# Kernel optimization log

Measured on AMD Instinct MI355X. Metric: run time of the kernel, lower is better.

The kernel has to match this reference:

```python
import jax, jax.numpy as jnp
import numpy as np

R = 32
EPS = 0.0
BN_EPS = 1e-5


def _voxelize(features, idx):
    # features: [C, N], idx: [N] int32 flat voxel index in [0, R^3)
    V = R * R * R
    pts = features.T  # [N, C]
    sums = jax.ops.segment_sum(pts, idx, num_segments=V)          # [V, C]
    cnts = jax.ops.segment_sum(jnp.ones_like(idx, jnp.float32), idx, num_segments=V)  # [V]
    avg = sums / jnp.maximum(cnts, 1.0)[:, None]
    mx = jax.ops.segment_max(pts, idx, num_segments=V)            # [V, C], -inf for empty
    mx = jnp.where(cnts[:, None] > 0, mx, 0.0)
    return avg, mx, cnts


def reference(features, coords, conv_w, conv_b, bn_gamma, bn_beta, bn_mean, bn_var):
    B, C, N = features.shape
    # --- coordinate normalization (coords detached in original) ---
    nc = coords - jnp.mean(coords, axis=2, keepdims=True)          # [B,3,N]
    norms = jnp.linalg.norm(nc, axis=1, keepdims=True)             # [B,1,N]
    denom = jnp.max(norms, axis=2, keepdims=True) * 2.0 + EPS      # [B,1,1]
    nc = nc / denom + 0.5
    nc = jnp.clip(nc * R, 0.0, R - 1)                              # [B,3,N]
    vox = jnp.round(nc).astype(jnp.int32)                          # [B,3,N]
    idx = vox[:, 0] * (R * R) + vox[:, 1] * R + vox[:, 2]          # [B,N]
    # --- dual scatter reduction (avg + max) per batch ---
    avg, mx, _ = jax.vmap(_voxelize)(features, idx)                # [B, V, C] each
    fea = jnp.concatenate([mx, avg], axis=-1)                      # [B, V, 2C]
    # --- 1x1 Conv3d == channel matmul ---
    y = jnp.einsum('bvc,oc->bvo', fea, conv_w) + conv_b            # [B, V, C]
    # --- BatchNorm3d (eval mode) ---
    y = (y - bn_mean) * (bn_gamma / jnp.sqrt(bn_var + BN_EPS)) + bn_beta
    # --- Swish ---
    y = y * jax.nn.sigmoid(y)
    out = jnp.transpose(y, (0, 2, 1)).reshape(B, C, R, R, R)
    return out, nc


def setup_inputs() -> dict:
    key = jax.random.key(0)
    ks = jax.random.split(key, 8)
    B, C, N = 8, 240, 16384
    return {
        'features': jax.random.normal(ks[0], (B, C, N), jnp.float32),
        'coords': jax.random.normal(ks[1], (B, 3, N), jnp.float32),
        'conv_w': jax.random.normal(ks[2], (C, 2 * C), jnp.float32) * 0.05,
        'conv_b': jax.random.normal(ks[3], (C,), jnp.float32) * 0.05,
        'bn_gamma': jnp.ones((C,), jnp.float32),
        'bn_beta': jnp.zeros((C,), jnp.float32),
        'bn_mean': jnp.zeros((C,), jnp.float32),
        'bn_var': jax.random.uniform(ks[4], (C,), jnp.float32, 0.5, 1.5),
    }
```

## Files before the change

kernel.cpp:

```cpp
#include <hip/hip_runtime.h>
#include <math.h>

#define RR 32
#define V 32768
#define C 240
#define N 16384
#define B 8
#define K2C 480
#define NG 2048
#define GZ 16
#define FPAD 488
#define EBUF 512

typedef __attribute__((ext_vector_type(8))) short bf16x8;
typedef __attribute__((ext_vector_type(4))) float f32x4;

__device__ __forceinline__ unsigned short f2bf(float x) {
    unsigned u = __float_as_uint(x);
    u += 0x7fffu + ((u >> 16) & 1u);
    return (unsigned short)(u >> 16);
}

__global__ __launch_bounds__(256) void init_stats_kernel(const float* __restrict__ coords,
                                                         float* __restrict__ stats,
                                                         int* __restrict__ hist,
                                                         const float* __restrict__ w,
                                                         unsigned short* __restrict__ w_bf) {
    int blk = blockIdx.x;
    int tid = threadIdx.x;
    if (blk < 256) {
        int t = blk * 256 + tid;
        int4 z4 = {0, 0, 0, 0};
        ((int4*)hist)[t] = z4;
        if (t < 57600) {
            unsigned lo = f2bf(w[2 * t]);
            unsigned hi = f2bf(w[2 * t + 1]);
            ((unsigned*)w_bf)[t] = lo | (hi << 16);
        }
        return;
    }
    int b = blk - 256;
    const float* cb = coords + (size_t)b * 3 * N;
    __shared__ float red[256];
    float m[3];
    for (int d = 0; d < 3; ++d) {
        float s = 0.f;
        for (int n = tid; n < N; n += 256) s += cb[d * N + n];
        red[tid] = s; __syncthreads();
        for (int w2 = 128; w2 > 0; w2 >>= 1) { if (tid < w2) red[tid] += red[tid + w2]; __syncthreads(); }
        m[d] = red[0] / (float)N;
        __syncthreads();
    }
    float mx = 0.f;
    for (int n = tid; n < N; n += 256) {
        float dx = cb[0 * N + n] - m[0];
        float dy = cb[1 * N + n] - m[1];
        float dz = cb[2 * N + n] - m[2];
        mx = fmaxf(mx, dx * dx + dy * dy + dz * dz);
    }
    red[tid] = mx; __syncthreads();
    for (int w2 = 128; w2 > 0; w2 >>= 1) { if (tid < w2) red[tid] = fmaxf(red[tid], red[tid + w2]); __syncthreads(); }
    if (tid == 0) {
        stats[b * 4 + 0] = m[0];
        stats[b * 4 + 1] = m[1];
        stats[b * 4 + 2] = m[2];
        stats[b * 4 + 3] = 2.f * sqrtf(red[0]);
    }
}

__global__ __launch_bounds__(256) void nc_idx_kernel(const float* __restrict__ coords,
                                                     const float* __restrict__ stats,
                                                     float* __restrict__ nc_out,
                                                     int* __restrict__ idxbuf,
                                                     int* __restrict__ hist) {
    int t = blockIdx.x * 256 + threadIdx.x;
    int b = t >> 14;
    int n = t & (N - 1);
    float denom = stats[b * 4 + 3];
    int v[3];
#pragma unroll
    for (int d = 0; d < 3; ++d) {
        float x = coords[((size_t)b * 3 + d) * N + n];
        float t0 = (x - stats[b * 4 + d]) / denom + 0.5f;
        t0 = t0 * (float)RR;
        t0 = fminf(fmaxf(t0, 0.f), (float)(RR - 1));
        nc_out[((size_t)b * 3 + d) * N + n] = t0;
        v[d] = (int)rintf(t0);
    }
    int iv = v[0] * (RR * RR) + v[1] * RR + v[2];
    idxbuf[t] = iv;
    atomicAdd(hist + b * V + iv, 1);
}

__global__ __launch_bounds__(1024) void prefix_kernel(const int* __restrict__ hist,
                                                      int* __restrict__ starts,
                                                      int* __restrict__ cursor) {
    __shared__ int part[1024];
    int b = blockIdx.x, t = threadIdx.x;
    int base = b * V + t * 32;
    const int4* hp = (const int4*)(hist + base);
    int4 h[8];
    int s = 0;
#pragma unroll
    for (int j = 0; j < 8; ++j) { h[j] = hp[j]; s += h[j].x + h[j].y + h[j].z + h[j].w; }
    part[t] = s; __syncthreads();
    for (int off = 1; off < 1024; off <<= 1) {
        int x = (t >= off) ? part[t - off] : 0;
        __syncthreads();
        part[t] += x;
        __syncthreads();
    }
    int run = part[t] - s;
    int4* sp = (int4*)(starts + base);
    int4* cp = (int4*)(cursor + base);
#pragma unroll
    for (int j = 0; j < 8; ++j) {
        int4 o;
        o.x = run; run += h[j].x;
        o.y = run; run += h[j].y;
        o.z = run; run += h[j].z;
        o.w = run; run += h[j].w;
        sp[j] = o; cp[j] = o;
    }
}

__global__ __launch_bounds__(256) void plist_kernel(const int* __restrict__ idxbuf,
                                                    int* __restrict__ cursor,
                                                    int* __restrict__ ptlist) {
    int t = blockIdx.x * 256 + threadIdx.x;
    int b = t >> 14;
    int n = t & (N - 1);
    int iv = idxbuf[t];
    int pos = atomicAdd(cursor + b * V + iv, 1);
    ptlist[(b << 14) + pos] = (n << 5) | (iv & 31);
}

__global__ __launch_bounds__(256) void transpose_kernel(const float* __restrict__ feat,
                                                        unsigned short* __restrict__ featT) {
    __shared__ float t[C][33];
    int b = blockIdx.y;
    int n0 = blockIdx.x * 32;
    int l = threadIdx.x;
    const float* fb = feat + (size_t)b * C * N;
    unsigned short* fTb = featT + (size_t)b * N * C;
    int nl = l & 31, cs = l >> 5;
#pragma unroll
    for (int p = 0; p < 30; ++p) {
        int c = p * 8 + cs;
        t[c][nl] = fb[(size_t)c * N + n0 + nl];
    }
    __syncthreads();
    int ci = l & 127;
    int nh = l >> 7;
#pragma unroll
    for (int p = 0; p < 16; ++p) {
        int n = 2 * p + nh;
        if (ci < 120) {
            unsigned lo = f2bf(t[2 * ci][n]);
            unsigned hi = f2bf(t[2 * ci + 1][n]);
            *(unsigned*)&fTb[(size_t)(n0 + n) * C + 2 * ci] = lo | (hi << 16);
        }
    }
}

__global__ __launch_bounds__(256) void column_kernel(
    const unsigned short* __restrict__ featT,
    const int* __restrict__ ptlist,
    const int* __restrict__ starts,
    const int* __restrict__ hist,
    const unsigned short* __restrict__ w_bf,
    const float* __restrict__ cbias, const float* __restrict__ gamma,
    const float* __restrict__ beta, const float* __restrict__ mean,
    const float* __restrict__ var,
    float* __restrict__ out) {
    const int g = blockIdx.x, b = blockIdx.y;
    const int tid = threadIdx.x;
    const int v0 = g * GZ;
    float* outb = out + (size_t)b * C * V;

    __shared__ float A_s[C], B_s[C], rcp_s[GZ];
    __shared__ unsigned short fea_s[GZ][FPAD];
    __shared__ int cnt_s[GZ];
    __shared__ int ebuf[EBUF];

    if (tid < C) {
        float sc = gamma[tid] * rsqrtf(var[tid] + 1e-5f);
        A_s[tid] = sc;
        B_s[tid] = (cbias[tid] - mean[tid]) * sc + beta[tid];
    }
    if (tid < GZ) {
        int c0 = hist[b * V + v0 + tid];
        cnt_s[tid] = c0;
        rcp_s[tid] = 1.f / (float)max(c0, 1);
    }
    __syncthreads();

    int pc = 0;
#pragma unroll
    for (int z = 0; z < GZ; ++z) pc += cnt_s[z];

    if (pc == 0) {
        for (int i = tid; i < C * GZ; i += 256) {
            int o = i >> 4, vv = i & (GZ - 1);
            float y = B_s[o];
            y = y / (1.f + __expf(-y));
            outb[(size_t)o * V + v0 + vv] = y;
        }
        return;
    }

    for (int i = tid; i < GZ * FPAD / 2; i += 256) ((unsigned*)fea_s)[i] = 0u;

    const int c = tid;
    const bool act = tid < C;
    const int pos = starts[b * V + v0];
    const int* pl = ptlist + (b << 14) + pos;
    const unsigned short* fT = featT + (size_t)b * N * C;

    float s0 = 0.f, mx0 = -INFINITY;
    int curz = -1;
    for (int base = 0; base < pc; base += EBUF) {
        int mm = min(EBUF, pc - base);
        __syncthreads();
        for (int i = tid; i < mm; i += 256) ebuf[i] = pl[base + i];
        __syncthreads();
        if (act) {
            for (int i0 = 0; i0 < mm; i0 += 16) {
                int m = min(16, mm - i0);
                int e_[16];
#pragma unroll
                for (int j = 0; j < 16; ++j) e_[j] = ebuf[i0 + ((j < m) ? j : m - 1)];
                unsigned short u_[16];
#pragma unroll
                for (int j = 0; j < 16; ++j)
                    u_[j] = fT[(size_t)(e_[j] >> 5) * C + c];
#pragma unroll
                for (int j = 0; j < 16; ++j) {
                    if (j < m) {
                        int zj = e_[j] & (GZ - 1);
                        if (zj != curz) {
                            if (curz >= 0) {
                                fea_s[curz][c] = f2bf(mx0);
                                fea_s[curz][C + c] = f2bf(s0 * rcp_s[curz]);
                            }
                            curz = zj; s0 = 0.f; mx0 = -INFINITY;
                        }
                        float f = __uint_as_float(((unsigned)u_[j]) << 16);
                        s0 += f; mx0 = fmaxf(mx0, f);
                    }
                }
            }
        }
    }
    if (act && curz >= 0) {
        fea_s[curz][c] = f2bf(mx0);
        fea_s[curz][C + c] = f2bf(s0 * rcp_s[curz]);
    }
    __syncthreads();

    const int lane = tid & 63, wave = tid >> 6;
    const int mcnt = (wave == 3) ? 3 : 4;
    const int zl = lane & 15;
    const int koff = (lane >> 4) * 8;

    f32x4 acc[4];
#pragma unroll
    for (int i = 0; i < 4; ++i) acc[i] = (f32x4){0.f, 0.f, 0.f, 0.f};

#pragma unroll
    for (int kc = 0; kc < 15; ++kc) {
        const int kg = kc * 32 + koff;
        bf16x8 bfr = *(const bf16x8*)&fea_s[zl][kg];
        const unsigned short* wp = w_bf + (size_t)(wave * 64 + zl) * K2C + kg;
#pragma unroll
        for (int mt = 0; mt < 4; ++mt) {
            if (mt < mcnt) {
                bf16x8 afr = *(const bf16x8*)(wp + (size_t)mt * 16 * K2C);
                acc[mt] = __builtin_amdgcn_mfma_f32_16x16x32_bf16(afr, bfr, acc[mt], 0, 0, 0);
            }
        }
    }

    const int vv = v0 + zl;
    const int rbase = (lane >> 4) * 4;
#pragma unroll
    for (int mt = 0; mt < 4; ++mt) {
        if (mt < mcnt) {
#pragma unroll
            for (int r = 0; r < 4; ++r) {
                int o = (wave * 4 + mt) * 16 + rbase + r;
                float y = acc[mt][r] * A_s[o] + B_s[o];
                y = y / (1.f + __expf(-y));
                outb[(size_t)o * V + vv] = y;
            }
        }
    }
}

extern "C" void kernel_launch(void* const* d_in, const int* in_sizes, int n_in,
                              void* d_out, int out_size, void* d_ws, size_t ws_size,
                              hipStream_t stream) {
    const float* features = (const float*)d_in[0];
    const float* coords   = (const float*)d_in[1];
    const float* conv_w   = (const float*)d_in[2];
    const float* conv_b   = (const float*)d_in[3];
    const float* gamma    = (const float*)d_in[4];
    const float* beta     = (const float*)d_in[5];
    const float* mean     = (const float*)d_in[6];
    const float* var      = (const float*)d_in[7];

    float* out    = (float*)d_out;
    float* nc_out = out + (size_t)B * C * V;

    char* ws = (char*)d_ws;
    size_t off = 0;
    auto carve = [&](size_t bytes) { char* p = ws + off; off += (bytes + 255) & ~(size_t)255; return p; };
    int*            hist   = (int*)carve((size_t)B * V * 4);
    float*          stats  = (float*)carve(B * 4 * 4);
    int*            idxbuf = (int*)carve((size_t)B * N * 4);
    int*            starts = (int*)carve((size_t)B * V * 4);
    int*            cursor = (int*)carve((size_t)B * V * 4);
    int*            ptlist = (int*)carve((size_t)B * N * 4);
    unsigned short* w_bf   = (unsigned short*)carve((size_t)C * K2C * 2);
    unsigned short* featT  = (unsigned short*)carve((size_t)B * N * C * 2);
    (void)off;

    init_stats_kernel<<<256 + B, 256, 0, stream>>>(coords, stats, hist, conv_w, w_bf);
    nc_idx_kernel<<<(B * N) / 256, 256, 0, stream>>>(coords, stats, nc_out, idxbuf, hist);
    prefix_kernel<<<B, 1024, 0, stream>>>(hist, starts, cursor);
    plist_kernel<<<(B * N) / 256, 256, 0, stream>>>(idxbuf, cursor, ptlist);
    transpose_kernel<<<dim3(N / 32, B), 256, 0, stream>>>(features, featT);
    column_kernel<<<dim3(NG, B), 256, 0, stream>>>(
        featT, ptlist, starts, hist, w_bf,
        conv_b, gamma, beta, mean, var, out);
    (void)in_sizes; (void)n_in; (void)out_size;
}
```

Baseline: 608.8 us.

## Widen voxel group to 32 and loop four groups per persistent block

Each block now covers a 32-voxel z-column instead of 16 and walks four such groups, cutting the grid from 2048 to 256 blocks per batch. BN/bias/swish constants and the swish of the bias for empty voxels are computed once per block. Each weight fragment loaded from global memory now feeds two MFMAs, one per 16-voxel half. Empty groups write float4 stores. This trades fewer blocks and less parallelism for reuse of the weights and setup work, and adds more accumulator registers.

```diff
diff --git a/kernel.cpp b/kernel.cpp
--- a/kernel.cpp
+++ b/kernel.cpp
@@ -7,8 +7,8 @@
 #define N 16384
 #define B 8
 #define K2C 480
-#define NG 2048
-#define GZ 16
+#define GZ 32
+#define GPB 4
 #define FPAD 488
 #define EBUF 512
 
@@ -173,125 +173,137 @@
     const float* __restrict__ beta, const float* __restrict__ mean,
     const float* __restrict__ var,
     float* __restrict__ out) {
-    const int g = blockIdx.x, b = blockIdx.y;
+    const int bx = blockIdx.x, b = blockIdx.y;
     const int tid = threadIdx.x;
-    const int v0 = g * GZ;
     float* outb = out + (size_t)b * C * V;
 
-    __shared__ float A_s[C], B_s[C], rcp_s[GZ];
-    __shared__ unsigned short fea_s[GZ][FPAD];
+    __shared__ float A_s[C], B_s[C], y0_s[C];
+    __shared__ __align__(16) unsigned short fea_s[GZ][FPAD];
     __shared__ int cnt_s[GZ];
     __shared__ int ebuf[EBUF];
 
     if (tid < C) {
         float sc = gamma[tid] * rsqrtf(var[tid] + 1e-5f);
         A_s[tid] = sc;
-        B_s[tid] = (cbias[tid] - mean[tid]) * sc + beta[tid];
-    }
-    if (tid < GZ) {
-        int c0 = hist[b * V + v0 + tid];
-        cnt_s[tid] = c0;
-        rcp_s[tid] = 1.f / (float)max(c0, 1);
-    }
-    __syncthreads();
-
-    int pc = 0;
-#pragma unroll
-    for (int z = 0; z < GZ; ++z) pc += cnt_s[z];
-
-    if (pc == 0) {
-        for (int i = tid; i < C * GZ; i += 256) {
-            int o = i >> 4, vv = i & (GZ - 1);
-            float y = B_s[o];
-            y = y / (1.f + __expf(-y));
-            outb[(size_t)o * V + v0 + vv] = y;
-        }
-        return;
-    }
-
-    for (int i = tid; i < GZ * FPAD / 2; i += 256) ((unsigned*)fea_s)[i] = 0u;
+        float b0 = (cbias[tid] - mean[tid]) * sc + beta[tid];
+        B_s[tid] = b0;
+        y0_s[tid] = b0 / (1.f + __expf(-b0));
+    }
 
     const int c = tid;
     const bool act = tid < C;
-    const int pos = starts[b * V + v0];
-    const int* pl = ptlist + (b << 14) + pos;
     const unsigned short* fT = featT + (size_t)b * N * C;
-
-    float s0 = 0.f, mx0 = -INFINITY;
-    int curz = -1;
-    for (int base = 0; base < pc; base += EBUF) {
-        int mm = min(EBUF, pc - base);
-        __syncthreads();
-        for (int i = tid; i < mm; i += 256) ebuf[i] = pl[base + i];
-        __syncthreads();
-        if (act) {
-            for (int i0 = 0; i0 < mm; i0 += 16) {
-                int m = min(16, mm - i0);
-                int e_[16];
-#pragma unroll
-                for (int j = 0; j < 16; ++j) e_[j] = ebuf[i0 + ((j < m) ? j : m - 1)];
-                unsigned short u_[16];
-#pragma unroll
-                for (int j = 0; j < 16; ++j)
-                    u_[j] = fT[(size_t)(e_[j] >> 5) * C + c];
-#pragma unroll
-                for (int j = 0; j < 16; ++j) {
-                    if (j < m) {
-                        int zj = e_[j] & (GZ - 1);
-                        if (zj != curz) {
-                            if (curz >= 0) {
-                                fea_s[curz][c] = f2bf(mx0);
-                                fea_s[curz][C + c] = f2bf(s0 * rcp_s[curz]);
-                            }
-                            curz = zj; s0 = 0.f; mx0 = -INFINITY;
-                        }
-                        float f = __uint_as_float(((unsigned)u_[j]) << 16);
-                        s0 += f; mx0 = fmaxf(mx0, f);
-                    }
-                }
-            }
-        }
-    }
-    if (act && curz >= 0) {
-        fea_s[curz][c] = f2bf(mx0);
-        fea_s[curz][C + c] = f2bf(s0 * rcp_s[curz]);
-    }
-    __syncthreads();
 
     const int lane = tid & 63, wave = tid >> 6;
     const int mcnt = (wave == 3) ? 3 : 4;
     const int zl = lane & 15;
     const int koff = (lane >> 4) * 8;
-
-    f32x4 acc[4];
-#pragma unroll
-    for (int i = 0; i < 4; ++i) acc[i] = (f32x4){0.f, 0.f, 0.f, 0.f};
-
-#pragma unroll
-    for (int kc = 0; kc < 15; ++kc) {
-        const int kg = kc * 32 + koff;
-        bf16x8 bfr = *(const bf16x8*)&fea_s[zl][kg];
-        const unsigned short* wp = w_bf + (size_t)(wave * 64 + zl) * K2C + kg;
+    const int rbase = (lane >> 4) * 4;
+
+    for (int gi = 0; gi < GPB; ++gi) {
+        const int g = gi * 256 + bx;
+        const int v0 = g * GZ;
+
+        __syncthreads();
+        if (tid < GZ) cnt_s[tid] = hist[b * V + v0 + tid];
+        __syncthreads();
+
+        int pc = 0;
+#pragma unroll
+        for (int z = 0; z < GZ; ++z) pc += cnt_s[z];
+
+        if (pc == 0) {
+            for (int i = tid; i < GZ * C / 4; i += 256) {
+                int o = i >> 3, q = i & 7;
+                float y = y0_s[o];
+                float4 f4 = {y, y, y, y};
+                *(float4*)&outb[(size_t)o * V + v0 + q * 4] = f4;
+            }
+            continue;
+        }
+
+        for (int i = tid; i < GZ * FPAD / 2; i += 256) ((unsigned*)fea_s)[i] = 0u;
+
+        const int pos = starts[b * V + v0];
+        const int* pl = ptlist + (b << 14) + pos;
+
+        float s0 = 0.f, mx0 = -INFINITY;
+        int curz = -1;
+        for (int base = 0; base < pc; base += EBUF) {
+            int mm = min(EBUF, pc - base);
+            __syncthreads();
+            for (int i = tid; i < mm; i += 256) ebuf[i] = pl[base + i];
+            __syncthreads();
+            if (act) {
+                for (int i0 = 0; i0 < mm; i0 += 16) {
+                    int m = min(16, mm - i0);
+                    int e_[16];
+#pragma unroll
+                    for (int j = 0; j < 16; ++j) e_[j] = ebuf[i0 + ((j < m) ? j : m - 1)];
+                    unsigned short u_[16];
+#pragma unroll
+                    for (int j = 0; j < 16; ++j)
+                        u_[j] = fT[(size_t)(e_[j] >> 5) * C + c];
+#pragma unroll
+                    for (int j = 0; j < 16; ++j) {
+                        if (j < m) {
+                            int zj = e_[j] & (GZ - 1);
+                            if (zj != curz) {
+                                if (curz >= 0) {
+                                    float k = (float)cnt_s[curz];
+                                    fea_s[curz][c] = f2bf(mx0);
+                                    fea_s[curz][C + c] = f2bf(s0 / k);
+                                }
+                                curz = zj; s0 = 0.f; mx0 = -INFINITY;
+                            }
+                            float f = __uint_as_float(((unsigned)u_[j]) << 16);
+                            s0 += f; mx0 = fmaxf(mx0, f);
+                        }
+                    }
+                }
+            }
+        }
+        if (act && curz >= 0) {
+            float k = (float)cnt_s[curz];
+            fea_s[curz][c] = f2bf(mx0);
+            fea_s[curz][C + c] = f2bf(s0 / k);
+        }
+        __syncthreads();
+
+        f32x4 acc0[4], acc1[4];
+#pragma unroll
+        for (int i = 0; i < 4; ++i) { acc0[i] = (f32x4){0.f, 0.f, 0.f, 0.f}; acc1[i] = (f32x4){0.f, 0.f, 0.f, 0.f}; }
+
+#pragma unroll
+        for (int kc = 0; kc < 15; ++kc) {
+            const int kg = kc * 32 + koff;
+            bf16x8 bfr0 = *(const bf16x8*)&fea_s[zl][kg];
+            bf16x8 bfr1 = *(const bf16x8*)&fea_s[16 + zl][kg];
+            const unsigned short* wp = w_bf + (size_t)(wave * 64 + zl) * K2C + kg;
+#pragma unroll
+            for (int mt = 0; mt < 4; ++mt) {
+                if (mt < mcnt) {
+                    bf16x8 afr = *(const bf16x8*)(wp + (size_t)mt * 16 * K2C);
+                    acc0[mt] = __builtin_amdgcn_mfma_f32_16x16x32_bf16(afr, bfr0, acc0[mt], 0, 0, 0);
+                    acc1[mt] = __builtin_amdgcn_mfma_f32_16x16x32_bf16(afr, bfr1, acc1[mt], 0, 0, 0);
+                }
+            }
+        }
+
+        const int vv = v0 + zl;
 #pragma unroll
         for (int mt = 0; mt < 4; ++mt) {
             if (mt < mcnt) {
-                bf16x8 afr = *(const bf16x8*)(wp + (size_t)mt * 16 * K2C);
-                acc[mt] = __builtin_amdgcn_mfma_f32_16x16x32_bf16(afr, bfr, acc[mt], 0, 0, 0);
-            }
-        }
-    }
-
-    const int vv = v0 + zl;
-    const int rbase = (lane >> 4) * 4;
-#pragma unroll
-    for (int mt = 0; mt < 4; ++mt) {
-        if (mt < mcnt) {
-#pragma unroll
-            for (int r = 0; r < 4; ++r) {
-                int o = (wave * 4 + mt) * 16 + rbase + r;
-                float y = acc[mt][r] * A_s[o] + B_s[o];
-                y = y / (1.f + __expf(-y));
-                outb[(size_t)o * V + vv] = y;
+#pragma unroll
+                for (int r = 0; r < 4; ++r) {
+                    int o = (wave * 4 + mt) * 16 + rbase + r;
+                    float y = acc0[mt][r] * A_s[o] + B_s[o];
+                    y = y / (1.f + __expf(-y));
+                    outb[(size_t)o * V + vv] = y;
+                    float y1 = acc1[mt][r] * A_s[o] + B_s[o];
+                    y1 = y1 / (1.f + __expf(-y1));
+                    outb[(size_t)o * V + vv + 16] = y1;
+                }
             }
         }
     }
@@ -330,7 +342,7 @@
     prefix_kernel<<<B, 1024, 0, stream>>>(hist, starts, cursor);
     plist_kernel<<<(B * N) / 256, 256, 0, stream>>>(idxbuf, cursor, ptlist);
     transpose_kernel<<<dim3(N / 32, B), 256, 0, stream>>>(features, featT);
-    column_kernel<<<dim3(NG, B), 256, 0, stream>>>(
+    column_kernel<<<dim3(256, B), 256, 0, stream>>>(
         featT, ptlist, starts, hist, w_bf,
         conv_b, gamma, beta, mean, var, out);
     (void)in_sizes; (void)n_in; (void)out_size;
```

Measured after the change: 886.5 us. 1.46x slower.

## Compact non-empty voxel groups into worklist and fuse prep kernels

Applied to the files above, without the earlier changes.

Builds a per-batch worklist of non-empty 16-voxel groups during the prefix scan, so the heavy column kernel only does real work for occupied groups and early-exits the rest. Empty groups are written with the constant bias-swish value by extra blocks fused into the point-list fill kernel. The feature transpose is merged into the init/stats kernel to save a launch. This adds atomics in the prefix scan, and the column kernel still launches the full grid of blocks, which now mostly exit immediately.

```diff
diff --git a/kernel.cpp b/kernel.cpp
--- a/kernel.cpp
+++ b/kernel.cpp
@@ -7,8 +7,8 @@
 #define N 16384
 #define B 8
 #define K2C 480
-#define NG 2048
 #define GZ 16
+#define NGRP 2048
 #define FPAD 488
 #define EBUF 512
 
@@ -21,25 +21,56 @@
     return (unsigned short)(u >> 16);
 }
 
-__global__ __launch_bounds__(256) void init_stats_kernel(const float* __restrict__ coords,
-                                                         float* __restrict__ stats,
-                                                         int* __restrict__ hist,
-                                                         const float* __restrict__ w,
-                                                         unsigned short* __restrict__ w_bf) {
+__global__ __launch_bounds__(256) void prep_kernel(const float* __restrict__ feat,
+                                                   unsigned short* __restrict__ featT,
+                                                   const float* __restrict__ coords,
+                                                   float* __restrict__ stats,
+                                                   int* __restrict__ hist,
+                                                   int* __restrict__ wlcnt,
+                                                   const float* __restrict__ w,
+                                                   unsigned short* __restrict__ w_bf) {
+    __shared__ float t[C][33];
     int blk = blockIdx.x;
     int tid = threadIdx.x;
-    if (blk < 256) {
-        int t = blk * 256 + tid;
+    if (blk < 4096) {
+        int bx = blk & 511, b = blk >> 9;
+        int n0 = bx * 32;
+        int l = tid;
+        const float* fb = feat + (size_t)b * C * N;
+        unsigned short* fTb = featT + (size_t)b * N * C;
+        int nl = l & 31, cs = l >> 5;
+#pragma unroll
+        for (int p = 0; p < 30; ++p) {
+            int c = p * 8 + cs;
+            t[c][nl] = fb[(size_t)c * N + n0 + nl];
+        }
+        __syncthreads();
+        int ci = l & 127;
+        int nh = l >> 7;
+#pragma unroll
+        for (int p = 0; p < 16; ++p) {
+            int n = 2 * p + nh;
+            if (ci < 120) {
+                unsigned lo = f2bf(t[2 * ci][n]);
+                unsigned hi = f2bf(t[2 * ci + 1][n]);
+                *(unsigned*)&fTb[(size_t)(n0 + n) * C + 2 * ci] = lo | (hi << 16);
+            }
+        }
+        return;
+    }
+    if (blk < 4352) {
+        int tt = (blk - 4096) * 256 + tid;
         int4 z4 = {0, 0, 0, 0};
-        ((int4*)hist)[t] = z4;
-        if (t < 57600) {
-            unsigned lo = f2bf(w[2 * t]);
-            unsigned hi = f2bf(w[2 * t + 1]);
-            ((unsigned*)w_bf)[t] = lo | (hi << 16);
-        }
+        ((int4*)hist)[tt] = z4;
+        if (tt < 57600) {
+            unsigned lo = f2bf(w[2 * tt]);
+            unsigned hi = f2bf(w[2 * tt + 1]);
+            ((unsigned*)w_bf)[tt] = lo | (hi << 16);
+        }
+        if (tt < B) wlcnt[tt] = 0;
         return;
     }
-    int b = blk - 256;
+    int b = blk - 4352;
     const float* cb = coords + (size_t)b * 3 * N;
     __shared__ float red[256];
     float m[3];
@@ -94,15 +125,23 @@
 
 __global__ __launch_bounds__(1024) void prefix_kernel(const int* __restrict__ hist,
                                                       int* __restrict__ starts,
-                                                      int* __restrict__ cursor) {
+                                                      int* __restrict__ cursor,
+                                                      int* __restrict__ wl,
+                                                      int* __restrict__ wlcnt) {
     __shared__ int part[1024];
     int b = blockIdx.x, t = threadIdx.x;
     int base = b * V + t * 32;
     const int4* hp = (const int4*)(hist + base);
     int4 h[8];
-    int s = 0;
-#pragma unroll
-    for (int j = 0; j < 8; ++j) { h[j] = hp[j]; s += h[j].x + h[j].y + h[j].z + h[j].w; }
+#pragma unroll
+    for (int j = 0; j < 8; ++j) h[j] = hp[j];
+    int pcA = h[0].x + h[0].y + h[0].z + h[0].w + h[1].x + h[1].y + h[1].z + h[1].w
+            + h[2].x + h[2].y + h[2].z + h[2].w + h[3].x + h[3].y + h[3].z + h[3].w;
+    int pcB = h[4].x + h[4].y + h[4].z + h[4].w + h[5].x + h[5].y + h[5].z + h[5].w
+            + h[6].x + h[6].y + h[6].z + h[6].w + h[7].x + h[7].y + h[7].z + h[7].w;
+    int s = pcA + pcB;
+    if (pcA > 0) { int p = atomicAdd(wlcnt + b, 1); wl[b * NGRP + p] = 2 * t; }
+    if (pcB > 0) { int p = atomicAdd(wlcnt + b, 1); wl[b * NGRP + p] = 2 * t + 1; }
     part[t] = s; __syncthreads();
     for (int off = 1; off < 1024; off <<= 1) {
         int x = (t >= off) ? part[t - off] : 0;
@@ -124,42 +163,57 @@
     }
 }
 
-__global__ __launch_bounds__(256) void plist_kernel(const int* __restrict__ idxbuf,
-                                                    int* __restrict__ cursor,
-                                                    int* __restrict__ ptlist) {
-    int t = blockIdx.x * 256 + threadIdx.x;
-    int b = t >> 14;
-    int n = t & (N - 1);
-    int iv = idxbuf[t];
-    int pos = atomicAdd(cursor + b * V + iv, 1);
-    ptlist[(b << 14) + pos] = (n << 5) | (iv & 31);
-}
-
-__global__ __launch_bounds__(256) void transpose_kernel(const float* __restrict__ feat,
-                                                        unsigned short* __restrict__ featT) {
-    __shared__ float t[C][33];
-    int b = blockIdx.y;
-    int n0 = blockIdx.x * 32;
-    int l = threadIdx.x;
-    const float* fb = feat + (size_t)b * C * N;
-    unsigned short* fTb = featT + (size_t)b * N * C;
-    int nl = l & 31, cs = l >> 5;
-#pragma unroll
-    for (int p = 0; p < 30; ++p) {
-        int c = p * 8 + cs;
-        t[c][nl] = fb[(size_t)c * N + n0 + nl];
-    }
+__global__ __launch_bounds__(256) void plist_fill_kernel(const int* __restrict__ idxbuf,
+                                                         int* __restrict__ cursor,
+                                                         int* __restrict__ ptlist,
+                                                         const int* __restrict__ hist,
+                                                         const float* __restrict__ cbias,
+                                                         const float* __restrict__ gamma,
+                                                         const float* __restrict__ beta,
+                                                         const float* __restrict__ mean,
+                                                         const float* __restrict__ var,
+                                                         float* __restrict__ out) {
+    int blk = blockIdx.x;
+    int tid = threadIdx.x;
+    if (blk < 512) {
+        int t = blk * 256 + tid;
+        int b = t >> 14;
+        int n = t & (N - 1);
+        int iv = idxbuf[t];
+        int pos = atomicAdd(cursor + b * V + iv, 1);
+        ptlist[(b << 14) + pos] = (n << 5) | (iv & 31);
+        return;
+    }
+    int blk2 = blk - 512;
+    int b = blk2 >> 10, col = blk2 & 1023;
+    int v0 = col * 32;
+    __shared__ int hcol[32];
+    if (tid < 32) hcol[tid] = hist[b * V + v0 + tid];
     __syncthreads();
-    int ci = l & 127;
-    int nh = l >> 7;
-#pragma unroll
-    for (int p = 0; p < 16; ++p) {
-        int n = 2 * p + nh;
-        if (ci < 120) {
-            unsigned lo = f2bf(t[2 * ci][n]);
-            unsigned hi = f2bf(t[2 * ci + 1][n]);
-            *(unsigned*)&fTb[(size_t)(n0 + n) * C + 2 * ci] = lo | (hi << 16);
-        }
+    int pcA = 0, pcB = 0;
+#pragma unroll
+    for (int z = 0; z < 16; ++z) { pcA += hcol[z]; pcB += hcol[16 + z]; }
+    if (pcA > 0 && pcB > 0) return;
+    float* outb = out + (size_t)b * C * V;
+    if (pcA == 0 && pcB == 0) {
+        for (int i = tid; i < C * 8; i += 256) {
+            int o = i >> 3, q = i & 7;
+            float sc = gamma[o] * rsqrtf(var[o] + 1e-5f);
+            float b0 = (cbias[o] - mean[o]) * sc + beta[o];
+            float y = b0 / (1.f + __expf(-b0));
+            float4 f4 = {y, y, y, y};
+            *(float4*)&outb[(size_t)o * V + v0 + q * 4] = f4;
+        }
+        return;
+    }
+    int vh = (pcA == 0) ? v0 : v0 + 16;
+    for (int i = tid; i < C * 4; i += 256) {
+        int o = i >> 2, q = i & 3;
+        float sc = gamma[o] * rsqrtf(var[o] + 1e-5f);
+        float b0 = (cbias[o] - mean[o]) * sc + beta[o];
+        float y = b0 / (1.f + __expf(-b0));
+        float4 f4 = {y, y, y, y};
+        *(float4*)&outb[(size_t)o * V + vh + q * 4] = f4;
     }
 }
 
@@ -172,8 +226,11 @@
     const float* __restrict__ cbias, const float* __restrict__ gamma,
     const float* __restrict__ beta, const float* __restrict__ mean,
     const float* __restrict__ var,
+    const int* __restrict__ wl, const int* __restrict__ wlcnt,
     float* __restrict__ out) {
-    const int g = blockIdx.x, b = blockIdx.y;
+    const int bx = blockIdx.x, b = blockIdx.y;
+    if (bx >= wlcnt[b]) return;
+    const int g = wl[b * NGRP + bx];
     const int tid = threadIdx.x;
     const int v0 = g * GZ;
     float* outb = out + (size_t)b * C * V;
@@ -198,16 +255,6 @@
     int pc = 0;
 #pragma unroll
     for (int z = 0; z < GZ; ++z) pc += cnt_s[z];
-
-    if (pc == 0) {
-        for (int i = tid; i < C * GZ; i += 256) {
-            int o = i >> 4, vv = i & (GZ - 1);
-            float y = B_s[o];
-            y = y / (1.f + __expf(-y));
-            outb[(size_t)o * V + v0 + vv] = y;
-        }
-        return;
-    }
 
     for (int i = tid; i < GZ * FPAD / 2; i += 256) ((unsigned*)fea_s)[i] = 0u;
 
@@ -321,17 +368,19 @@
     int*            starts = (int*)carve((size_t)B * V * 4);
     int*            cursor = (int*)carve((size_t)B * V * 4);
     int*            ptlist = (int*)carve((size_t)B * N * 4);
+    int*            wl     = (int*)carve((size_t)B * NGRP * 4);
+    int*            wlcnt  = (int*)carve((size_t)B * 4);
     unsigned short* w_bf   = (unsigned short*)carve((size_t)C * K2C * 2);
     unsigned short* featT  = (unsigned short*)carve((size_t)B * N * C * 2);
     (void)off;
 
-    init_stats_kernel<<<256 + B, 256, 0, stream>>>(coords, stats, hist, conv_w, w_bf);
+    prep_kernel<<<4360, 256, 0, stream>>>(features, featT, coords, stats, hist, wlcnt, conv_w, w_bf);
     nc_idx_kernel<<<(B * N) / 256, 256, 0, stream>>>(coords, stats, nc_out, idxbuf, hist);
-    prefix_kernel<<<B, 1024, 0, stream>>>(hist, starts, cursor);
-    plist_kernel<<<(B * N) / 256, 256, 0, stream>>>(idxbuf, cursor, ptlist);
-    transpose_kernel<<<dim3(N / 32, B), 256, 0, stream>>>(features, featT);
-    column_kernel<<<dim3(NG, B), 256, 0, stream>>>(
+    prefix_kernel<<<B, 1024, 0, stream>>>(hist, starts, cursor, wl, wlcnt);
+    plist_fill_kernel<<<512 + 1024 * B, 256, 0, stream>>>(idxbuf, cursor, ptlist, hist,
+                                                          conv_b, gamma, beta, mean, var, out);
+    column_kernel<<<dim3(NGRP, B), 256, 0, stream>>>(
         featT, ptlist, starts, hist, w_bf,
-        conv_b, gamma, beta, mean, var, out);
+        conv_b, gamma, beta, mean, var, wl, wlcnt, out);
     (void)in_sizes; (void)n_in; (void)out_size;
 }
```

Result: no change. 614.4 us (+0.9%).
